# Kernel optimization log

Measured on AMD Instinct MI355X. Metric: run time of the kernel, lower is better.

The kernel has to match this reference:

```python
import jax, jax.numpy as jnp
import numpy as np

B, S, H, R = 32, 512, 1024, 64


def _bernoulli(key, shape, p=0.05):
    return (jax.random.uniform(key, shape) < p).astype(jnp.float32)


def setup_inputs() -> dict:
    key = jax.random.key(0)
    ks = jax.random.split(key, 16)
    context = jax.random.normal(ks[0], (B, S, H), dtype=jnp.float32)
    masks = jnp.ones((B, S), dtype=jnp.float32)
    all_subject_heads = _bernoulli(ks[1], (B, S))
    all_subject_tails = _bernoulli(ks[2], (B, S))
    # one-hot subject head/tail positions (tail >= head)
    h_pos = jax.random.randint(ks[3], (B,), 0, S // 2)
    t_pos = h_pos + jax.random.randint(ks[4], (B,), 0, 8)
    subject_head = jax.nn.one_hot(h_pos, S, dtype=jnp.float32)
    subject_tail = jax.nn.one_hot(t_pos, S, dtype=jnp.float32)
    object_heads = _bernoulli(ks[5], (B, S, R))
    object_tails = _bernoulli(ks[6], (B, S, R))
    # learned parameters (PyTorch Linear: y = x @ W.T + b; store as [in, out])
    sc = 1.0 / np.sqrt(H)
    Ws_h = jax.random.uniform(ks[7], (H, 1), minval=-sc, maxval=sc)
    bs_h = jnp.zeros((1,), dtype=jnp.float32)
    Ws_t = jax.random.uniform(ks[8], (H, 1), minval=-sc, maxval=sc)
    bs_t = jnp.zeros((1,), dtype=jnp.float32)
    Wo_h = jax.random.uniform(ks[9], (H, R), minval=-sc, maxval=sc)
    bo_h = jnp.zeros((R,), dtype=jnp.float32)
    Wo_t = jax.random.uniform(ks[10], (H, R), minval=-sc, maxval=sc)
    bo_t = jnp.zeros((R,), dtype=jnp.float32)
    return dict(context=context, masks=masks,
                all_subject_heads=all_subject_heads, all_subject_tails=all_subject_tails,
                subject_head=subject_head, subject_tail=subject_tail,
                object_heads=object_heads, object_tails=object_tails,
                Ws_h=Ws_h, bs_h=bs_h, Ws_t=Ws_t, bs_t=bs_t,
                Wo_h=Wo_h, bo_h=bo_h, Wo_t=Wo_t, bo_t=bo_t)


def _bce_with_logits(logits, targets):
    # numerically stable, matches F.binary_cross_entropy_with_logits(reduction='none')
    return jnp.maximum(logits, 0.0) - logits * targets + jnp.log1p(jnp.exp(-jnp.abs(logits)))


def _masked_loss(gold, pred, mask):
    loss = _bce_with_logits(pred, gold)
    if loss.ndim != mask.ndim:
        mask = mask[..., None]
    return jnp.sum(loss * mask) / jnp.sum(mask)


def reference(context, masks, all_subject_heads, all_subject_tails,
              subject_head, subject_tail, object_heads, object_tails,
              Ws_h, bs_h, Ws_t, bs_t, Wo_h, bo_h, Wo_t, bo_t):
    # subject logits: [B,S]
    pred_subject_heads = (context @ Ws_h + bs_h)[..., 0]
    pred_subject_tails = (context @ Ws_t + bs_t)[..., 0]
    # subject pooling: one-hot [B,S] x context [B,S,H] -> [B,H]
    sub_h = jnp.einsum('bs,bsh->bh', subject_head, context)
    sub_t = jnp.einsum('bs,bsh->bh', subject_tail, context)
    subject = (sub_h + sub_t) * 0.5
    context_subject = context + subject[:, None, :]  # [B,S,H]
    pred_object_heads = context_subject @ Wo_h + bo_h  # [B,S,R]
    pred_object_tails = context_subject @ Wo_t + bo_t  # [B,S,R]
    loss = (_masked_loss(all_subject_heads, pred_subject_heads, masks)
            + _masked_loss(all_subject_tails, pred_subject_tails, masks)
            + _masked_loss(object_heads, pred_object_heads, masks)
            + _masked_loss(object_tails, pred_object_tails, masks))
    return loss
```

## Files before the change

kernel.cpp:

```cpp
#include <hip/hip_runtime.h>


#define B_  32
#define S_  512
#define H_  1024
#define R_  64
#define M_  (B_ * S_)
#define NPAD 160
#define NVALID 130
#define BK 64
#define BKP 72
#define MT 32
#define NCHUNK (H_ / BK)
#define TBLK 20
#define NTHR 640

typedef __attribute__((ext_vector_type(4))) float  floatx4;
typedef __attribute__((ext_vector_type(8))) short  short8;
typedef __attribute__((ext_vector_type(4))) unsigned short u16x4;
typedef __attribute__((ext_vector_type(8))) unsigned short u16x8;

__device__ __forceinline__ unsigned short f2bf(float f) {
    unsigned int u = __float_as_uint(f);
    u = (u + 0x7FFFu + ((u >> 16) & 1u)) >> 16;
    return (unsigned short)u;
}

__device__ __forceinline__ void gload_lds16(const unsigned short* g, unsigned short* l) {
    __builtin_amdgcn_global_load_lds(
        (const __attribute__((address_space(1))) unsigned int*)g,
        (__attribute__((address_space(3))) unsigned int*)l, 16, 0, 0);
}

__global__ __launch_bounds__(256) void aux_kernel(
        const float* __restrict__ ctx, const float* __restrict__ head,
        const float* __restrict__ tail, const float* __restrict__ masks,
        const float* __restrict__ Wo_h, const float* __restrict__ Wo_t,
        const float* __restrict__ Ws_h, const float* __restrict__ Ws_t,
        const float* __restrict__ bo_h, const float* __restrict__ bo_t,
        const float* __restrict__ bs_h, const float* __restrict__ bs_t,
        unsigned short* __restrict__ WtG, float* __restrict__ rowBias,
        float* __restrict__ accum) {
    const int tid = threadIdx.x;
    __shared__ float tr[32][257];
    __shared__ float subj[H_];
    __shared__ float partS[4][256];
    __shared__ int cnt;
    __shared__ int   sidx[8];
    __shared__ float sw[8];

    if (blockIdx.x < TBLK) {
        const int kt = blockIdx.x / 5, nt = blockIdx.x % 5;
        const int k0 = kt * 256, n0 = nt * 32;
        if (n0 < 128) {
            const float* src = (n0 < 64) ? Wo_h : Wo_t;
            const int cb = n0 & 63;
            const int nn = tid & 31, kk = tid >> 5;
#pragma unroll
            for (int i = 0; i < 32; ++i) {
                const int k = k0 + i * 8 + kk;
                tr[nn][i * 8 + kk] = src[(size_t)k * R_ + cb + nn];
            }
            __syncthreads();
#pragma unroll
            for (int p = 0; p < 4; ++p) {
                const int chunk = p * 256 + tid;
                const int n = chunk >> 5;
                const int kc = (chunk & 31) * 8;
                u16x8 v;
#pragma unroll
                for (int j = 0; j < 8; ++j) v[j] = f2bf(tr[n][kc + j]);
                *(u16x8*)(WtG + (size_t)(n0 + n) * H_ + k0 + kc) = v;
            }
        } else {
#pragma unroll
            for (int p = 0; p < 4; ++p) {
                const int chunk = p * 256 + tid;
                const int n = 128 + (chunk >> 5);
                const int kc = (chunk & 31) * 8;
                u16x8 v;
#pragma unroll
                for (int j = 0; j < 8; ++j) {
                    float f = (n == 128) ? Ws_h[k0 + kc + j]
                            : (n == 129) ? Ws_t[k0 + kc + j] : 0.0f;
                    v[j] = f2bf(f);
                }
                *(u16x8*)(WtG + (size_t)n * H_ + k0 + kc) = v;
            }
        }
        return;
    }

    const int b = blockIdx.x - TBLK;
    if (tid == 0) cnt = 0;
    __syncthreads();
    float msk = 0.0f;
    for (int s = tid; s < S_; s += 256) {
        float w = 0.5f * (head[b * S_ + s] + tail[b * S_ + s]);
        if (w != 0.0f) {
            int i = atomicAdd(&cnt, 1);
            if (i < 8) { sidx[i] = s; sw[i] = w; }
        }
        msk += masks[b * S_ + s];
    }
    for (int o = 32; o > 0; o >>= 1) msk += __shfl_down(msk, o, 64);
    if ((tid & 63) == 0) atomicAdd(&accum[1], msk);
    __syncthreads();
    const int nnz = cnt < 8 ? cnt : 8;
    for (int h = tid; h < H_; h += 256) {
        float a = 0.0f;
        for (int i = 0; i < nnz; i++)
            a += sw[i] * ctx[((size_t)b * S_ + sidx[i]) * H_ + h];
        subj[h] = a;
    }
    __syncthreads();
    {
        const int cg = tid & 31;
        const int ks = tid >> 5;
        const int c4 = cg * 4;
        const float* W = (c4 < 64) ? Wo_h : Wo_t;
        const int cc = c4 & 63;
        const int kk0 = ks * 128;
        float ax = 0.f, ay = 0.f, az = 0.f, aw = 0.f;
#pragma unroll 4
        for (int k = kk0; k < kk0 + 128; ++k) {
            const float4 w = *(const float4*)(W + (size_t)k * R_ + cc);
            const float sv = subj[k];
            ax += sv * w.x; ay += sv * w.y; az += sv * w.z; aw += sv * w.w;
        }
        partS[0][tid] = ax; partS[1][tid] = ay;
        partS[2][tid] = az; partS[3][tid] = aw;
    }
    __syncthreads();
    if (tid < NPAD) {
        float bias = tid < 64  ? bo_h[tid]
                   : tid < 128 ? bo_t[tid - 64]
                   : tid == 128 ? bs_h[0]
                   : tid == 129 ? bs_t[0] : 0.0f;
        float a2 = 0.0f;
        if (tid < 128) {
            const int g = tid >> 2, j = tid & 3;
#pragma unroll
            for (int s = 0; s < 8; ++s) a2 += partS[j][s * 32 + g];
        }
        rowBias[b * NPAD + tid] = bias + a2;
    }
}

__global__ __launch_bounds__(NTHR, 4) void main_kernel(
        const float* __restrict__ ctx, const unsigned short* __restrict__ WtG,
        const float* __restrict__ rowBias, const float* __restrict__ masks,
        const float* __restrict__ ash, const float* __restrict__ ast,
        const float* __restrict__ oh, const float* __restrict__ ot,
        float* __restrict__ accum, float* __restrict__ out) {
    __shared__ __align__(16) unsigned short Asm[2][MT * BKP];
    __shared__ __align__(16) unsigned short Bsm[2][NPAD * BK];
    __shared__ float rbuf[10];

    const int tid  = threadIdx.x;
    const int gm0  = blockIdx.x * MT;
    const int b    = gm0 >> 9;
    const int wave = tid >> 6, lane = tid & 63;
    const int wm = wave & 1;
    const int wn = wave >> 1;
    const int lr = lane & 15, q = lane >> 4;

    const int ar = tid >> 4, af = tid & 15;
    const bool aAct = tid < 512;
    const float* aSrc = ctx + (size_t)(gm0 + ar) * H_ + af * 4;
    unsigned short* aD0 = &Asm[0][ar * BKP + af * 4];
    unsigned short* aD1 = &Asm[1][ar * BKP + af * 4];

    const int br = tid >> 3, bc = (tid & 7) * 16;
    const int bswz = bc ^ ((br & 7) << 4);
    const unsigned short* bSrc = WtG + (size_t)br * H_ + (bswz >> 1);
    const int bDstOff = br * 64 + (bc >> 1);

    const int aOff = (wm * 16 + lr) * BKP + q * 8;
    int bOff[2];
#pragma unroll
    for (int tt = 0; tt < 2; ++tt) {
        const int row = wn * 32 + tt * 16 + lr;
        bOff[tt] = row * 128 + ((q * 16) ^ ((row & 7) << 4));
    }

    floatx4 acc[2];
#pragma unroll
    for (int tt = 0; tt < 2; ++tt) acc[tt] = (floatx4){0.f, 0.f, 0.f, 0.f};

    {
        float4 v0;
        if (aAct) v0 = *(const float4*)(aSrc);
#pragma unroll
        for (int p = 0; p < 2; ++p)
            gload_lds16(bSrc + (size_t)p * 80 * H_, &Bsm[0][p * 5120 + bDstOff]);
        if (aAct) {
            u16x4 u0 = { f2bf(v0.x), f2bf(v0.y), f2bf(v0.z), f2bf(v0.w) };
            *(u16x4*)aD0 = u0;
        }
    }
    __syncthreads();

    int cur = 0;
    for (int t = 0; t < NCHUNK; ++t) {
        const int nk = (t + 1) * BK;
        float4 v0;
        if (t < NCHUNK - 1) {
            if (aAct) v0 = *(const float4*)(aSrc + nk);
            unsigned short* bN = &Bsm[cur ^ 1][0];
#pragma unroll
            for (int p = 0; p < 2; ++p)
                gload_lds16(bSrc + (size_t)p * 80 * H_ + nk, bN + p * 5120 + bDstOff);
        }
        const unsigned short* Ac = &Asm[cur][0];
        const char* Bc = (const char*)&Bsm[cur][0];
#pragma unroll
        for (int kk = 0; kk < BK; kk += 32) {
            short8 afr = *(const short8*)&Ac[aOff + kk];
#pragma unroll
            for (int tt = 0; tt < 2; ++tt) {
                short8 bfr = *(const short8*)(Bc + (bOff[tt] ^ (kk << 1)));
                acc[tt] = __builtin_amdgcn_mfma_f32_16x16x32_bf16(afr, bfr, acc[tt], 0, 0, 0);
            }
        }
        if (t < NCHUNK - 1) {
            if (aAct) {
                u16x4 u0 = { f2bf(v0.x), f2bf(v0.y), f2bf(v0.z), f2bf(v0.w) };
                *(u16x4*)(cur ? aD0 : aD1) = u0;
            }
            __syncthreads();
            cur ^= 1;
        }
    }

    float lsum = 0.0f;
#pragma unroll
    for (int tt = 0; tt < 2; ++tt) {
        const int col = wn * 32 + tt * 16 + lr;
        if (col < NVALID) {
            const float rb = rowBias[b * NPAD + col];
#pragma unroll
            for (int i = 0; i < 4; ++i) {
                const int row = gm0 + wm * 16 + q * 4 + i;
                const float l = acc[tt][i] + rb;
                float tgt;
                if (col < 64)        tgt = oh[(size_t)row * R_ + col];
                else if (col < 128)  tgt = ot[(size_t)row * R_ + (col - 64)];
                else if (col == 128) tgt = ash[row];
                else                 tgt = ast[row];
                const float mk = masks[row];
                const float bce = fmaxf(l, 0.0f) - l * tgt + log1pf(__expf(-fabsf(l)));
                lsum += bce * mk;
            }
        }
    }
    for (int o = 32; o > 0; o >>= 1) lsum += __shfl_down(lsum, o, 64);
    if (lane == 0) rbuf[wave] = lsum;
    __syncthreads();
    if (tid == 0) {
        float s0 = 0.0f;
#pragma unroll
        for (int w = 0; w < 10; ++w) s0 += rbuf[w];
        atomicAdd(&accum[0], s0);
        __threadfence();
        const unsigned int prev = atomicAdd((unsigned int*)(accum + 2), 1u);
        if (prev == gridDim.x - 1) {
            const float s = atomicAdd(&accum[0], 0.0f);
            const float m = atomicAdd(&accum[1], 0.0f);
            out[0] = s / m;
        }
    }
}

extern "C" void kernel_launch(void* const* d_in, const int* in_sizes, int n_in,
                              void* d_out, int out_size, void* d_ws, size_t ws_size,
                              hipStream_t stream) {
    const float* ctx   = (const float*)d_in[0];
    const float* masks = (const float*)d_in[1];
    const float* ash   = (const float*)d_in[2];
    const float* ast   = (const float*)d_in[3];
    const float* sh    = (const float*)d_in[4];
    const float* st    = (const float*)d_in[5];
    const float* oh    = (const float*)d_in[6];
    const float* ot    = (const float*)d_in[7];
    const float* Ws_h  = (const float*)d_in[8];
    const float* bs_h  = (const float*)d_in[9];
    const float* Ws_t  = (const float*)d_in[10];
    const float* bs_t  = (const float*)d_in[11];
    const float* Wo_h  = (const float*)d_in[12];
    const float* bo_h  = (const float*)d_in[13];
    const float* Wo_t  = (const float*)d_in[14];
    const float* bo_t  = (const float*)d_in[15];
    float* out = (float*)d_out;

    char* ws = (char*)d_ws;
    float* accum   = (float*)(ws + 0);
    float* rowBias = (float*)(ws + 256);
    unsigned short* WtG = (unsigned short*)(ws + 256 + 32 * NPAD * 4);

    hipMemsetAsync(accum, 0, 12, stream);
    aux_kernel<<<TBLK + B_, 256, 0, stream>>>(ctx, sh, st, masks, Wo_h, Wo_t,
                                              Ws_h, Ws_t, bo_h, bo_t, bs_h, bs_t,
                                              WtG, rowBias, accum);
    main_kernel<<<M_ / MT, NTHR, 0, stream>>>(ctx, WtG, rowBias, masks,
                                              ash, ast, oh, ot, accum, out);
}
```

Measured before the change: 167.4 us.

## Stream fp32 A tiles to LDS asynchronously and convert to bf16 at fragment load

The A operand (context) now goes straight from global memory into a swizzled fp32 LDS buffer through global_load_lds, replacing the register round-trip that converted to bf16 before the LDS store. The bf16 conversion moves to the MFMA fragment read. The pipeline is rebuilt with explicit vmcnt/lgkmcnt waits and raw barriers so the next stage's loads can overlap compute. Launch bounds are raised to five blocks per CU. In exchange the A buffer doubles in LDS size, and conversion work is repeated per wave that reads the same rows.

```diff
diff --git a/kernel.cpp b/kernel.cpp
--- a/kernel.cpp
+++ b/kernel.cpp
@@ -9,7 +9,6 @@
 #define NPAD 160
 #define NVALID 130
 #define BK 64
-#define BKP 72
 #define MT 32
 #define NCHUNK (H_ / BK)
 #define TBLK 20
@@ -26,7 +25,14 @@
     return (unsigned short)u;
 }
 
-__device__ __forceinline__ void gload_lds16(const unsigned short* g, unsigned short* l) {
+__device__ __forceinline__ short8 cvt8(float4 a, float4 b) {
+    union { unsigned short us[8]; short8 s8; } u;
+    u.us[0] = f2bf(a.x); u.us[1] = f2bf(a.y); u.us[2] = f2bf(a.z); u.us[3] = f2bf(a.w);
+    u.us[4] = f2bf(b.x); u.us[5] = f2bf(b.y); u.us[6] = f2bf(b.z); u.us[7] = f2bf(b.w);
+    return u.s8;
+}
+
+__device__ __forceinline__ void gload16(const void* g, void* l) {
     __builtin_amdgcn_global_load_lds(
         (const __attribute__((address_space(1))) unsigned int*)g,
         (__attribute__((address_space(3))) unsigned int*)l, 16, 0, 0);
@@ -121,15 +127,15 @@
         const float* W = (c4 < 64) ? Wo_h : Wo_t;
         const int cc = c4 & 63;
         const int kk0 = ks * 128;
-        float ax = 0.f, ay = 0.f, az = 0.f, aw = 0.f;
+        float ax = 0.f, ay = 0.f, az = 0.f, aw2 = 0.f;
 #pragma unroll 4
         for (int k = kk0; k < kk0 + 128; ++k) {
             const float4 w = *(const float4*)(W + (size_t)k * R_ + cc);
             const float sv = subj[k];
-            ax += sv * w.x; ay += sv * w.y; az += sv * w.z; aw += sv * w.w;
+            ax += sv * w.x; ay += sv * w.y; az += sv * w.z; aw2 += sv * w.w;
         }
         partS[0][tid] = ax; partS[1][tid] = ay;
-        partS[2][tid] = az; partS[3][tid] = aw;
+        partS[2][tid] = az; partS[3][tid] = aw2;
     }
     __syncthreads();
     if (tid < NPAD) {
@@ -147,13 +153,13 @@
     }
 }
 
-__global__ __launch_bounds__(NTHR, 4) void main_kernel(
+__global__ __launch_bounds__(NTHR, 5) void main_kernel(
         const float* __restrict__ ctx, const unsigned short* __restrict__ WtG,
         const float* __restrict__ rowBias, const float* __restrict__ masks,
         const float* __restrict__ ash, const float* __restrict__ ast,
         const float* __restrict__ oh, const float* __restrict__ ot,
         float* __restrict__ accum, float* __restrict__ out) {
-    __shared__ __align__(16) unsigned short Asm[2][MT * BKP];
+    __shared__ __align__(16) float          AsmF[2][MT * BK];
     __shared__ __align__(16) unsigned short Bsm[2][NPAD * BK];
     __shared__ float rbuf[10];
 
@@ -165,18 +171,20 @@
     const int wn = wave >> 1;
     const int lr = lane & 15, q = lane >> 4;
 
-    const int ar = tid >> 4, af = tid & 15;
-    const bool aAct = tid < 512;
-    const float* aSrc = ctx + (size_t)(gm0 + ar) * H_ + af * 4;
-    unsigned short* aD0 = &Asm[0][ar * BKP + af * 4];
-    unsigned short* aD1 = &Asm[1][ar * BKP + af * 4];
+    const bool aw = (tid < 512);
+    const int  as_  = tid & 511;
+    const int  arow = as_ >> 4;
+    const float* aSrcG = ctx + (size_t)(gm0 + arow) * H_
+                       + (((((as_ & 15) * 16)) ^ ((arow & 7) << 4)) >> 2);
+    const int  aDstF = arow * BK + (as_ & 15) * 4;
 
     const int br = tid >> 3, bc = (tid & 7) * 16;
-    const int bswz = bc ^ ((br & 7) << 4);
-    const unsigned short* bSrc = WtG + (size_t)br * H_ + (bswz >> 1);
-    const int bDstOff = br * 64 + (bc >> 1);
-
-    const int aOff = (wm * 16 + lr) * BKP + q * 8;
+    const unsigned short* bSrcG = WtG + (size_t)br * H_ + ((bc ^ ((br & 7) << 4)) >> 1);
+    const int bDstS = br * BK + (bc >> 1);
+
+    const int aRow  = wm * 16 + lr;
+    const int aBase = aRow * 256;
+    const int aSw   = (aRow & 7) << 4;
     int bOff[2];
 #pragma unroll
     for (int tt = 0; tt < 2; ++tt) {
@@ -188,50 +196,46 @@
 #pragma unroll
     for (int tt = 0; tt < 2; ++tt) acc[tt] = (floatx4){0.f, 0.f, 0.f, 0.f};
 
-    {
-        float4 v0;
-        if (aAct) v0 = *(const float4*)(aSrc);
-#pragma unroll
-        for (int p = 0; p < 2; ++p)
-            gload_lds16(bSrc + (size_t)p * 80 * H_, &Bsm[0][p * 5120 + bDstOff]);
-        if (aAct) {
-            u16x4 u0 = { f2bf(v0.x), f2bf(v0.y), f2bf(v0.z), f2bf(v0.w) };
-            *(u16x4*)aD0 = u0;
-        }
-    }
-    __syncthreads();
-
-    int cur = 0;
-    for (int t = 0; t < NCHUNK; ++t) {
-        const int nk = (t + 1) * BK;
-        float4 v0;
-        if (t < NCHUNK - 1) {
-            if (aAct) v0 = *(const float4*)(aSrc + nk);
-            unsigned short* bN = &Bsm[cur ^ 1][0];
-#pragma unroll
-            for (int p = 0; p < 2; ++p)
-                gload_lds16(bSrc + (size_t)p * 80 * H_ + nk, bN + p * 5120 + bDstOff);
-        }
-        const unsigned short* Ac = &Asm[cur][0];
-        const char* Bc = (const char*)&Bsm[cur][0];
-#pragma unroll
-        for (int kk = 0; kk < BK; kk += 32) {
-            short8 afr = *(const short8*)&Ac[aOff + kk];
-#pragma unroll
-            for (int tt = 0; tt < 2; ++tt) {
-                short8 bfr = *(const short8*)(Bc + (bOff[tt] ^ (kk << 1)));
-                acc[tt] = __builtin_amdgcn_mfma_f32_16x16x32_bf16(afr, bfr, acc[tt], 0, 0, 0);
-            }
-        }
-        if (t < NCHUNK - 1) {
-            if (aAct) {
-                u16x4 u0 = { f2bf(v0.x), f2bf(v0.y), f2bf(v0.z), f2bf(v0.w) };
-                *(u16x4*)(cur ? aD0 : aD1) = u0;
-            }
-            __syncthreads();
-            cur ^= 1;
-        }
-    }
+#define STAGE(bufi, koff) do {                                                 \
+        gload16(bSrcG + (koff), &Bsm[bufi][bDstS]);                            \
+        gload16(bSrcG + 80 * H_ + (koff), &Bsm[bufi][5120 + bDstS]);           \
+        if (aw) gload16(aSrcG + (koff), &AsmF[bufi][aDstF]);                   \
+    } while (0)
+
+#define COMPUTE(bufi) do {                                                     \
+        const char* Acp = (const char*)&AsmF[bufi][0];                         \
+        const char* Bcp = (const char*)&Bsm[bufi][0];                          \
+        _Pragma("unroll")                                                      \
+        for (int kk = 0; kk < BK; kk += 32) {                                  \
+            const int ia = kk * 4 + q * 32;                                    \
+            const float4 f0 = *(const float4*)(Acp + aBase + (ia ^ aSw));      \
+            const float4 f1 = *(const float4*)(Acp + aBase + ((ia + 16) ^ aSw));\
+            const short8 afr = cvt8(f0, f1);                                   \
+            _Pragma("unroll")                                                  \
+            for (int tt = 0; tt < 2; ++tt) {                                   \
+                const short8 bfr = *(const short8*)(Bcp + (bOff[tt] ^ (kk << 1)));\
+                acc[tt] = __builtin_amdgcn_mfma_f32_16x16x32_bf16(afr, bfr, acc[tt], 0, 0, 0);\
+            }                                                                  \
+        }                                                                      \
+    } while (0)
+
+    STAGE(0, 0);
+
+    for (int t = 0; t < NCHUNK - 1; ++t) {
+        const int cur = t & 1;
+        STAGE(cur ^ 1, (t + 1) * BK);
+        if (aw) asm volatile("s_waitcnt vmcnt(3)" ::: "memory");
+        else    asm volatile("s_waitcnt vmcnt(2)" ::: "memory");
+        __builtin_amdgcn_s_barrier();
+        __builtin_amdgcn_sched_barrier(0);
+        COMPUTE(cur);
+        asm volatile("s_waitcnt lgkmcnt(0)" ::: "memory");
+        __builtin_amdgcn_s_barrier();
+    }
+    asm volatile("s_waitcnt vmcnt(0)" ::: "memory");
+    __builtin_amdgcn_s_barrier();
+    __builtin_amdgcn_sched_barrier(0);
+    COMPUTE((NCHUNK - 1) & 1);
 
     float lsum = 0.0f;
 #pragma unroll
@@ -270,6 +274,8 @@
             out[0] = s / m;
         }
     }
+#undef STAGE
+#undef COMPUTE
 }
 
 extern "C" void kernel_launch(void* const* d_in, const int* in_sizes, int n_in,
```

Result: slower. 174.0 us (+3.9%).
